# Performance work log

Measured on AMD Instinct MI355X. Metric: run time of the kernel, lower is better.

The kernel has to match this reference:

```python
import jax, jax.numpy as jnp
import numpy as np

HID, E, S, L_CAP, EPS = 768, 1536, 128, 512, 1e-5


def _rope_seq(x):
    """RoPE along axis 1. x: [b, n, 2, s]."""
    n, s = x.shape[1], x.shape[-1]
    half = s // 2
    inv_freq = jnp.power(10000.0, -jnp.arange(half, dtype=x.dtype) / half)  # [half]
    sinusoid = jnp.arange(n, dtype=x.dtype)[:, None, None] * inv_freq       # [n,1,half]
    sin, cos = jnp.sin(sinusoid), jnp.cos(sinusoid)
    x1, x2 = jnp.split(x, 2, axis=-1)
    return jnp.concatenate([x1 * cos - x2 * sin, x2 * cos + x1 * sin], axis=-1)


def setup_inputs() -> dict:
    key = jax.random.key(0)
    ks = jax.random.split(key, 6)
    B, L = 32, 512
    return {
        "x": jax.random.normal(ks[0], (B, L, HID), dtype=jnp.float32),
        "ln_gamma": jnp.ones((HID,), jnp.float32),
        "ln_beta": jnp.zeros((HID,), jnp.float32),
        "uv_W": jax.random.normal(ks[1], (HID, 2 * E + S), jnp.float32) * 0.02,
        "uv_b": jnp.zeros((2 * E + S,), jnp.float32),
        "gamma_qk": jax.random.normal(ks[2], (2, S), jnp.float32) * 0.02,
        "beta_qk": jnp.zeros((2, S), jnp.float32),
        "w_rel": jax.random.normal(ks[3], (2 * L_CAP - 1,), jnp.float32) * 0.02,
        "o_W": jax.random.normal(ks[4], (E, HID), jnp.float32) * 0.02,
        "o_b": jnp.zeros((HID,), jnp.float32),
    }


def reference(x, ln_gamma, ln_beta, uv_W, uv_b, gamma_qk, beta_qk, w_rel, o_W, o_b):
    L = x.shape[1]
    shortcut = x
    # LayerNorm
    mu = jnp.mean(x, axis=-1, keepdims=True)
    var = jnp.mean(jnp.square(x - mu), axis=-1, keepdims=True)
    xn = (x - mu) * jax.lax.rsqrt(var + EPS) * ln_gamma + ln_beta
    # uv projection + silu, split into u, v, base
    uv = jax.nn.silu(xn @ uv_W + uv_b)                       # [b, n, 2e+s]
    u, v, base = jnp.split(uv, [E, 2 * E], axis=-1)          # [b,n,e], [b,n,e], [b,n,s]
    # per-head affine then RoPE -> q, k
    base = base[..., None, :] * gamma_qk + beta_qk           # [b, n, 2, s]
    base = _rope_seq(base)
    q, k = base[..., 0, :], base[..., 1, :]
    # relu^2 attention kernel with Toeplitz relative position bias
    qk = jnp.einsum('bnd,bmd->bnm', q, k)
    idx = jnp.arange(L)
    bias = w_rel[idx[None, :] - idx[:, None] + L - 1]        # bias[i,j] = w[j-i+L-1]
    kernel = jnp.square(jax.nn.relu(qk / L + bias))
    # gated value aggregation + output projection + residual
    out = u * jnp.einsum('bnm,bme->bne', kernel, v)
    out = out @ o_W + o_b
    return out + shortcut
```

## Files before the change

kernel.cpp:

```cpp
#include <hip/hip_runtime.h>
#include <hip/hip_bf16.h>
#include <math.h>

typedef __bf16 bf16x8 __attribute__((ext_vector_type(8)));
typedef float f32x4 __attribute__((ext_vector_type(4)));
typedef unsigned short u16x4 __attribute__((ext_vector_type(4)));

#define AS1P const __attribute__((address_space(1))) void*
#define AS3P __attribute__((address_space(3))) void*

__device__ __forceinline__ float b2f(unsigned short h) {
    unsigned int u = ((unsigned int)h) << 16;
    return __builtin_bit_cast(float, u);
}
__device__ __forceinline__ unsigned short f2b(float f) {
    unsigned int u = __builtin_bit_cast(unsigned int, f);
    u += 0x7FFFu + ((u >> 16) & 1u);
    return (unsigned short)(u >> 16);
}
__device__ __forceinline__ float silu(float c) {
    return c * __builtin_amdgcn_rcpf(1.0f + __expf(-c));
}

__global__ __launch_bounds__(256) void k_convT(const float* __restrict__ src,
                                               unsigned short* __restrict__ dst,
                                               int R, int C) {
    __shared__ float tile[32][33];
    int tx = threadIdx.x, ty = threadIdx.y;
    int r0 = blockIdx.y << 5, c0 = blockIdx.x << 5;
#pragma unroll
    for (int i = 0; i < 4; ++i)
        tile[ty + 8 * i][tx] = src[(long long)(r0 + ty + 8 * i) * C + c0 + tx];
    __syncthreads();
#pragma unroll
    for (int i = 0; i < 4; ++i)
        dst[(long long)(c0 + ty + 8 * i) * R + r0 + tx] = f2b(tile[tx][ty + 8 * i]);
}

__global__ __launch_bounds__(256) void k_ln(const float* __restrict__ x,
                                            const float* __restrict__ g,
                                            const float* __restrict__ b,
                                            unsigned short* __restrict__ xn) {
    int row = blockIdx.x;
    int t = threadIdx.x;
    const float* xr = x + (long long)row * 768;
    float v0 = xr[t], v1 = xr[t + 256], v2 = xr[t + 512];
    float s = v0 + v1 + v2;
    float q = v0 * v0 + v1 * v1 + v2 * v2;
#pragma unroll
    for (int off = 32; off > 0; off >>= 1) {
        s += __shfl_xor(s, off);
        q += __shfl_xor(q, off);
    }
    __shared__ float ss[4], sq[4];
    int w = t >> 6;
    if ((t & 63) == 0) { ss[w] = s; sq[w] = q; }
    __syncthreads();
    float S_ = ss[0] + ss[1] + ss[2] + ss[3];
    float Q_ = sq[0] + sq[1] + sq[2] + sq[3];
    float mu = S_ * (1.0f / 768.0f);
    float var = Q_ * (1.0f / 768.0f) - mu * mu;
    float rs = rsqrtf(var + 1e-5f);
    unsigned short* xo = xn + (long long)row * 768;
    xo[t]       = f2b((v0 - mu) * rs * g[t]       + b[t]);
    xo[t + 256] = f2b((v1 - mu) * rs * g[t + 256] + b[t + 256]);
    xo[t + 512] = f2b((v2 - mu) * rs * g[t + 512] + b[t + 512]);
}

__global__ __launch_bounds__(128) void k_rope(const unsigned short* __restrict__ bS,
                                              const float* __restrict__ gqk,
                                              const float* __restrict__ bqk,
                                              unsigned short* __restrict__ q,
                                              unsigned short* __restrict__ k) {
    int row = blockIdx.x;
    int l = row & 511;
    int s = threadIdx.x;
    int j = s & 63;
    int partner = s ^ 64;
    float b0 = b2f(bS[(long long)row * 128 + s]);
    float bp = b2f(bS[(long long)row * 128 + partner]);
    float invf = __expf((float)j * -0.14391156831f);
    float th = (float)l * invf;
    float sn, cs;
    __sincosf(th, &sn, &cs);
    float sign = (s < 64) ? -1.0f : 1.0f;
    float preq  = b0 * gqk[s]           + bqk[s];
    float preqp = bp * gqk[partner]     + bqk[partner];
    q[(long long)row * 128 + s] = f2b(preq * cs + sign * preqp * sn);
    float prek  = b0 * gqk[128 + s]       + bqk[128 + s];
    float prekp = bp * gqk[128 + partner] + bqk[128 + partner];
    k[(long long)row * 128 + s] = f2b(prek * cs + sign * prekp * sn);
}

__global__ __launch_bounds__(256) void k_qk(const unsigned short* __restrict__ A,
                                            const unsigned short* __restrict__ B,
                                            const float* __restrict__ wrel,
                                            unsigned short* __restrict__ P) {
    __shared__ __align__(16) unsigned short As[128 * 64];
    __shared__ __align__(16) unsigned short Bs[128 * 64];
    int t = threadIdx.x;
    int w = t >> 6, lane = t & 63;
    int wr = w >> 1, wc = w & 1;
    int bx = blockIdx.x, by = blockIdx.y, bz = blockIdx.z;
    const unsigned short* Ab = A + (long long)bz * 512 * 128 + (long long)by * 128 * 128;
    const unsigned short* Bb = B + (long long)bz * 512 * 128 + (long long)bx * 128 * 128;

    f32x4 acc[4][4];
#pragma unroll
    for (int m = 0; m < 4; ++m)
#pragma unroll
        for (int n = 0; n < 4; ++n) acc[m][n] = (f32x4){0.f, 0.f, 0.f, 0.f};

    int rowA = (w << 3) + (lane >> 3);
    int colA = (lane & 7) << 3;

    for (int k0 = 0; k0 < 128; k0 += 64) {
#pragma unroll
        for (int i = 0; i < 4; ++i) {
            int r = (i << 5) + rowA;
            __builtin_amdgcn_global_load_lds(
                (AS1P)(Ab + (long long)r * 128 + k0 + colA),
                (AS3P)(&As[(i << 11) + (w << 9)]), 16, 0, 0);
            __builtin_amdgcn_global_load_lds(
                (AS1P)(Bb + (long long)r * 128 + k0 + colA),
                (AS3P)(&Bs[(i << 11) + (w << 9)]), 16, 0, 0);
        }
        __syncthreads();
#pragma unroll
        for (int ks = 0; ks < 2; ++ks) {
            bf16x8 af[4], bfr[4];
#pragma unroll
            for (int m = 0; m < 4; ++m)
                af[m] = *(const bf16x8*)&As[((wr << 6) + (m << 4) + (lane & 15)) * 64 +
                                            (ks << 5) + ((lane >> 4) << 3)];
#pragma unroll
            for (int n = 0; n < 4; ++n)
                bfr[n] = *(const bf16x8*)&Bs[((wc << 6) + (n << 4) + (lane & 15)) * 64 +
                                             (ks << 5) + ((lane >> 4) << 3)];
#pragma unroll
            for (int m = 0; m < 4; ++m)
#pragma unroll
                for (int n = 0; n < 4; ++n)
                    acc[m][n] = __builtin_amdgcn_mfma_f32_16x16x32_bf16(bfr[n], af[m],
                                                                        acc[m][n], 0, 0, 0);
        }
        __syncthreads();
    }

    int c15 = lane & 15, qq = lane >> 4;
    int rowb = (by << 7) + (wr << 6) + c15;
    int colb = (bx << 7) + (wc << 6) + (qq << 2);
#pragma unroll
    for (int m = 0; m < 4; ++m) {
#pragma unroll
        for (int n = 0; n < 4; ++n) {
            int grow = rowb + (m << 4);
            int gcol = colb + (n << 4);
            f32x4 a = acc[m][n];
            int base = gcol - grow + 511;
            u16x4 o;
#pragma unroll
            for (int i = 0; i < 4; ++i) {
                float val = a[i] * (1.0f / 512.0f) + wrel[base + i];
                val = fmaxf(val, 0.0f);
                o[i] = f2b(val * val);
            }
            *(u16x4*)(P + ((long long)(bz * 512 + grow)) * 512 + gcol) = o;
        }
    }
}

__device__ __forceinline__ bf16x8 ldsread(const unsigned short* p) {
    bf16x8 r;
    unsigned int off =
        (unsigned int)(unsigned long long)(__attribute__((address_space(3))) const void*)p;
    asm volatile("ds_read_b128 %0, %1" : "=v"(r) : "v"(off));
    return r;
}
__device__ __forceinline__ bf16x8 frag32(const unsigned short* tile, int r, int qq) {
    return ldsread(tile + r * 32 + ((qq ^ ((r >> 1) & 3)) << 3));
}
template <int ROWS, int K>
__device__ __forceinline__ void stage_t(const unsigned short* __restrict__ g,
                                        unsigned short* lds, int t) {
#pragma unroll
    for (int i = 0; i < ROWS / 64; ++i) {
        int slot = t + (i << 8);
        int row = slot >> 2;
        int gs = (slot & 3) ^ ((row >> 1) & 3);
        __builtin_amdgcn_global_load_lds(
            (AS1P)(g + (long long)row * K + (gs << 3)),
            (AS3P)(lds + slot * 8), 16, 0, 0);
    }
}

template <bool SWAP, int NT>
__device__ __forceinline__ void ring_kloop(const unsigned short* __restrict__ Ab,
                                           const unsigned short* __restrict__ Bb,
                                           unsigned short* As, unsigned short* Bs,
                                           f32x4 (&acc)[8][4], int t, int wc, int c15, int qq) {
    constexpr int K = NT * 32;
    constexpr int ASLOT = 128 * 32, BSLOT = 256 * 32;
    stage_t<128, K>(Ab, As, t);
    stage_t<256, K>(Bb, Bs, t);
    stage_t<128, K>(Ab + 32, As + ASLOT, t);
    stage_t<256, K>(Bb + 32, Bs + BSLOT, t);
    int slot = 0;
    for (int kt = 0; kt < NT; ++kt) {
        if (kt < NT - 1)
            asm volatile("s_waitcnt vmcnt(6)" ::: "memory");
        else
            asm volatile("s_waitcnt vmcnt(0)" ::: "memory");
        __builtin_amdgcn_s_barrier();
        __builtin_amdgcn_sched_barrier(0);
        if (kt + 2 < NT) {
            int ns = slot + 2;
            if (ns >= 3) ns -= 3;
            stage_t<128, K>(Ab + (long long)(kt + 2) * 32, As + ns * ASLOT, t);
            stage_t<256, K>(Bb + (long long)(kt + 2) * 32, Bs + ns * BSLOT, t);
        }
        const unsigned short* At = As + slot * ASLOT;
        const unsigned short* Bt = Bs + slot * BSLOT;
        bf16x8 af[8], bfr[4];
#pragma unroll
        for (int n = 0; n < 4; ++n) bfr[n] = frag32(Bt, wc * 64 + n * 16 + c15, qq);
#pragma unroll
        for (int m = 0; m < 8; ++m) af[m] = frag32(At, m * 16 + c15, qq);
        asm volatile("s_waitcnt lgkmcnt(0)" ::: "memory");
        __builtin_amdgcn_sched_barrier(0);
        __builtin_amdgcn_s_setprio(1);
#pragma unroll
        for (int m = 0; m < 8; ++m)
#pragma unroll
            for (int n = 0; n < 4; ++n) {
                if constexpr (SWAP)
                    acc[m][n] = __builtin_amdgcn_mfma_f32_16x16x32_bf16(bfr[n], af[m],
                                                                        acc[m][n], 0, 0, 0);
                else
                    acc[m][n] = __builtin_amdgcn_mfma_f32_16x16x32_bf16(af[m], bfr[n],
                                                                        acc[m][n], 0, 0, 0);
            }
        __builtin_amdgcn_s_setprio(0);
        slot = (slot + 1 == 3) ? 0 : slot + 1;
    }
}

template <int EPI, bool SWZ, int NT>
__global__ __launch_bounds__(256, 2) void k_ring(const unsigned short* __restrict__ A,
                                                 const unsigned short* __restrict__ B,
                                                 long long strideA, long long strideB,
                                                 void* p0, void* p1, void* p2,
                                                 const void* p3) {
    constexpr int K = NT * 32;
    __shared__ __align__(16) unsigned short As[3][128 * 32];
    __shared__ __align__(16) unsigned short Bs[3][256 * 32];
    int t = threadIdx.x;
    int w = t >> 6, lane = t & 63;
    int wc = w, c15 = lane & 15, qq = lane >> 4;
    int bx = blockIdx.x, by = blockIdx.y, bz = blockIdx.z;
    if constexpr (SWZ) {
        int gx = gridDim.x;
        int nb = gx * gridDim.y;
        int bid = by * gx + bx;
        int s = (bid & 7) * (nb >> 3) + (bid >> 3);
        bx = s % gx;
        by = s / gx;
    }
    const unsigned short* Ab = A + bz * strideA + (long long)by * 128 * K;
    const unsigned short* Bb = B + bz * strideB + (long long)bx * 256 * K;

    f32x4 acc[8][4];
#pragma unroll
    for (int m = 0; m < 8; ++m)
#pragma unroll
        for (int n = 0; n < 4; ++n) acc[m][n] = (f32x4){0.f, 0.f, 0.f, 0.f};

    bool swapped = true;
    if constexpr (EPI == 10) {
        swapped = !(bx >= 6 && bx < 12);
        if (swapped)
            ring_kloop<true, NT>(Ab, Bb, &As[0][0], &Bs[0][0], acc, t, wc, c15, qq);
        else
            ring_kloop<false, NT>(Ab, Bb, &As[0][0], &Bs[0][0], acc, t, wc, c15, qq);
    } else {
        ring_kloop<true, NT>(Ab, Bb, &As[0][0], &Bs[0][0], acc, t, wc, c15, qq);
    }

    if constexpr (EPI == 10) {
        if (swapped) {
            int rowb = by * 128 + c15;
            int colb = bx * 256 + wc * 64 + (qq << 2);
#pragma unroll
            for (int m = 0; m < 8; ++m) {
#pragma unroll
                for (int n = 0; n < 4; ++n) {
                    int R = rowb + m * 16;
                    int C = colb + n * 16;
                    f32x4 a = acc[m][n];
                    if (C < 1536) {
                        f32x4 bb = *(const f32x4*)((const float*)p3 + C);
                        u16x4 o;
#pragma unroll
                        for (int i = 0; i < 4; ++i) o[i] = f2b(silu(a[i] + bb[i]));
                        *(u16x4*)((unsigned short*)p0 + (long long)R * 1536 + C) = o;
                    } else if (C < 3200) {
                        f32x4 bb = *(const f32x4*)((const float*)p3 + C);
                        u16x4 o;
#pragma unroll
                        for (int i = 0; i < 4; ++i) o[i] = f2b(silu(a[i] + bb[i]));
                        *(u16x4*)((unsigned short*)p2 + (long long)R * 128 + (C - 3072)) = o;
                    }
                }
            }
        } else {
            int rowb = by * 128 + (qq << 2);
            int colb = bx * 256 + wc * 64 + c15;
#pragma unroll
            for (int m = 0; m < 8; ++m) {
#pragma unroll
                for (int n = 0; n < 4; ++n) {
                    int R = rowb + m * 16;
                    int C = colb + n * 16;
                    float bias = ((const float*)p3)[C];
                    f32x4 a = acc[m][n];
                    u16x4 o;
#pragma unroll
                    for (int i = 0; i < 4; ++i) o[i] = f2b(silu(a[i] + bias));
                    int bb2 = R >> 9, mm = R & 511;
                    *(u16x4*)((unsigned short*)p1 +
                              ((long long)bb2 * 1536 + (C - 1536)) * 512 + mm) = o;
                }
            }
        }
    } else if constexpr (EPI == 2) {
        int rowb = by * 128 + c15;
        int colb = bx * 256 + wc * 64 + (qq << 2);
#pragma unroll
        for (int m = 0; m < 8; ++m) {
#pragma unroll
            for (int n = 0; n < 4; ++n) {
                int R = rowb + m * 16;
                int C = colb + n * 16;
                f32x4 a = acc[m][n];
                long long idx = ((long long)(bz * 512 + R)) * 1536 + C;
                u16x4 uu = *(const u16x4*)((const unsigned short*)p1 + idx);
                u16x4 o;
#pragma unroll
                for (int i = 0; i < 4; ++i) o[i] = f2b(a[i] * b2f(uu[i]));
                *(u16x4*)((unsigned short*)p0 + idx) = o;
            }
        }
    } else {
        int rowb = by * 128 + c15;
        int colb = bx * 256 + wc * 64 + (qq << 2);
#pragma unroll
        for (int m = 0; m < 8; ++m) {
#pragma unroll
            for (int n = 0; n < 4; ++n) {
                int R = rowb + m * 16;
                int C = colb + n * 16;
                f32x4 a = acc[m][n];
                long long idx = (long long)R * 768 + C;
                f32x4 xv = *(const f32x4*)((const float*)p2 + idx);
                f32x4 ob = *(const f32x4*)((const float*)p1 + C);
                f32x4 o;
#pragma unroll
                for (int i = 0; i < 4; ++i) o[i] = a[i] + ob[i] + xv[i];
                *(f32x4*)((float*)p0 + idx) = o;
            }
        }
    }
}

extern "C" void kernel_launch(void* const* d_in, const int* in_sizes, int n_in,
                              void* d_out, int out_size, void* d_ws, size_t ws_size,
                              hipStream_t stream) {
    const float* x     = (const float*)d_in[0];
    const float* ln_g  = (const float*)d_in[1];
    const float* ln_b  = (const float*)d_in[2];
    const float* uv_W  = (const float*)d_in[3];
    const float* uv_b  = (const float*)d_in[4];
    const float* g_qk  = (const float*)d_in[5];
    const float* b_qk  = (const float*)d_in[6];
    const float* w_rel = (const float*)d_in[7];
    const float* o_W   = (const float*)d_in[8];
    const float* o_b   = (const float*)d_in[9];
    float* out = (float*)d_out;

    char* ws = (char*)d_ws;
    size_t off = 0;
    auto alloc = [&](size_t bytes) {
        void* p = ws + off;
        off += (bytes + 255) & ~(size_t)255;
        return p;
    };
    unsigned short* uvWT = (unsigned short*)alloc(3200ll * 768 * 2);
    unsigned short* oWT  = (unsigned short*)alloc(768ll * 1536 * 2);
    unsigned short* xn   = (unsigned short*)alloc(16384ll * 768 * 2);
    unsigned short* u    = (unsigned short*)alloc(16384ll * 1536 * 2);
    unsigned short* vT   = (unsigned short*)alloc(32ll * 1536 * 512 * 2);
    unsigned short* bS   = (unsigned short*)alloc(16384ll * 128 * 2);
    unsigned short* q    = (unsigned short*)alloc(32ll * 512 * 128 * 2);
    unsigned short* k    = (unsigned short*)alloc(32ll * 512 * 128 * 2);
    unsigned short* P     = xn;
    unsigned short* gated = u;

    k_convT<<<dim3(100, 24), dim3(32, 8), 0, stream>>>(uv_W, uvWT, 768, 3200);
    k_convT<<<dim3(24, 48), dim3(32, 8), 0, stream>>>(o_W, oWT, 1536, 768);
    k_ln<<<16384, 256, 0, stream>>>(x, ln_g, ln_b, xn);
    k_ring<10, true, 24><<<dim3(13, 128), 256, 0, stream>>>(
        xn, uvWT, 0, 0, (void*)u, (void*)vT, (void*)bS, (const void*)uv_b);
    k_rope<<<16384, 128, 0, stream>>>(bS, g_qk, b_qk, q, k);
    k_qk<<<dim3(4, 4, 32), 256, 0, stream>>>(q, k, w_rel, P);
    k_ring<2, false, 16><<<dim3(6, 4, 32), 256, 0, stream>>>(
        P, vT, 512ll * 512, 1536ll * 512, (void*)gated, (void*)u, nullptr, nullptr);
    k_ring<3, true, 48><<<dim3(3, 128), 256, 0, stream>>>(
        gated, oWT, 0, 0, (void*)out, (void*)o_b, (void*)x, nullptr);
}
```

Baseline: 296.7 us.

## Switch GEMMs to 256x256 tiles with 8 waves and half-tile double-buffered staging

Measured after the change: 291.8 us. About the same (-1.7%).

```diff
diff --git a/kernel.cpp b/kernel.cpp
--- a/kernel.cpp
+++ b/kernel.cpp
@@ -177,86 +177,115 @@
     asm volatile("ds_read_b128 %0, %1" : "=v"(r) : "v"(off));
     return r;
 }
-__device__ __forceinline__ bf16x8 frag32(const unsigned short* tile, int r, int qq) {
-    return ldsread(tile + r * 32 + ((qq ^ ((r >> 1) & 3)) << 3));
-}
-template <int ROWS, int K>
-__device__ __forceinline__ void stage_t(const unsigned short* __restrict__ g,
-                                        unsigned short* lds, int t) {
-#pragma unroll
-    for (int i = 0; i < ROWS / 64; ++i) {
-        int slot = t + (i << 8);
+__device__ __forceinline__ void stage_half(const unsigned short* __restrict__ g, int ldk,
+                                           unsigned short* lds, int t) {
+#pragma unroll
+    for (int i = 0; i < 2; ++i) {
+        int slot = t + (i << 9);
         int row = slot >> 2;
-        int gs = (slot & 3) ^ ((row >> 1) & 3);
+        int gs = (slot & 3) ^ ((slot >> 3) & 3);
         __builtin_amdgcn_global_load_lds(
-            (AS1P)(g + (long long)row * K + (gs << 3)),
+            (AS1P)(g + (long long)row * ldk + (gs << 3)),
             (AS3P)(lds + slot * 8), 16, 0, 0);
     }
 }
 
 template <bool SWAP, int NT>
-__device__ __forceinline__ void ring_kloop(const unsigned short* __restrict__ Ab,
-                                           const unsigned short* __restrict__ Bb,
-                                           unsigned short* As, unsigned short* Bs,
-                                           f32x4 (&acc)[8][4], int t, int wc, int c15, int qq) {
-    constexpr int K = NT * 32;
-    constexpr int ASLOT = 128 * 32, BSLOT = 256 * 32;
-    stage_t<128, K>(Ab, As, t);
-    stage_t<256, K>(Bb, Bs, t);
-    stage_t<128, K>(Ab + 32, As + ASLOT, t);
-    stage_t<256, K>(Bb + 32, Bs + BSLOT, t);
-    int slot = 0;
-    for (int kt = 0; kt < NT; ++kt) {
-        if (kt < NT - 1)
-            asm volatile("s_waitcnt vmcnt(6)" ::: "memory");
-        else
-            asm volatile("s_waitcnt vmcnt(0)" ::: "memory");
-        __builtin_amdgcn_s_barrier();
-        __builtin_amdgcn_sched_barrier(0);
-        if (kt + 2 < NT) {
-            int ns = slot + 2;
-            if (ns >= 3) ns -= 3;
-            stage_t<128, K>(Ab + (long long)(kt + 2) * 32, As + ns * ASLOT, t);
-            stage_t<256, K>(Bb + (long long)(kt + 2) * 32, Bs + ns * BSLOT, t);
-        }
-        const unsigned short* At = As + slot * ASLOT;
-        const unsigned short* Bt = Bs + slot * BSLOT;
-        bf16x8 af[8], bfr[4];
-#pragma unroll
-        for (int n = 0; n < 4; ++n) bfr[n] = frag32(Bt, wc * 64 + n * 16 + c15, qq);
-#pragma unroll
-        for (int m = 0; m < 8; ++m) af[m] = frag32(At, m * 16 + c15, qq);
-        asm volatile("s_waitcnt lgkmcnt(0)" ::: "memory");
-        __builtin_amdgcn_sched_barrier(0);
-        __builtin_amdgcn_s_setprio(1);
-#pragma unroll
-        for (int m = 0; m < 8; ++m)
-#pragma unroll
-            for (int n = 0; n < 4; ++n) {
-                if constexpr (SWAP)
-                    acc[m][n] = __builtin_amdgcn_mfma_f32_16x16x32_bf16(bfr[n], af[m],
-                                                                        acc[m][n], 0, 0, 0);
+__device__ __forceinline__ void kloop8(const unsigned short* __restrict__ Ab,
+                                       const unsigned short* __restrict__ Bb,
+                                       unsigned short* As, unsigned short* Bs,
+                                       f32x4 (&acc)[8][4], int tid,
+                                       int wr, int wc, int c15, int qq, int gq) {
+    constexpr int K = NT * 64;
+    stage_half(Ab, K, As + 0, tid);
+    stage_half(Bb, K, Bs + 0, tid);
+    stage_half(Ab + 32, K, As + 8192, tid);
+    stage_half(Bb + 32, K, Bs + 8192, tid);
+    stage_half(Ab + 64, K, As + 16384, tid);
+    stage_half(Bb + 64, K, Bs + 16384, tid);
+    asm volatile("s_waitcnt vmcnt(8)" ::: "memory");
+    __builtin_amdgcn_s_barrier();
+
+    bf16x8 bfr[4], af[4];
+    for (int t = 0; t < NT; ++t) {
+        const int b = t & 1;
+        const unsigned short* A0 = As + b * 16384;
+        const unsigned short* B0 = Bs + b * 16384;
+#pragma unroll
+        for (int p = 0; p < 4; ++p) {
+            const int ks = p >> 1, mh = p & 1;
+            const unsigned short* At = A0 + ks * 8192;
+            const unsigned short* Bt = B0 + ks * 8192;
+            if (mh == 0) {
+#pragma unroll
+                for (int n = 0; n < 4; ++n)
+                    bfr[n] = ldsread(Bt + (wc * 64 + n * 16 + c15) * 32 + gq * 8);
+            }
+#pragma unroll
+            for (int j = 0; j < 4; ++j)
+                af[j] = ldsread(At + (wr * 128 + (mh * 4 + j) * 16 + c15) * 32 + gq * 8);
+            if (p == 0) {
+                if (t + 1 < NT)
+                    stage_half(Ab + (t + 1) * 64 + 32, K,
+                               As + (((t + 1) & 1) * 2 + 1) * 8192, tid);
+            } else if (p == 1) {
+                if (t + 1 < NT)
+                    stage_half(Bb + (t + 1) * 64 + 32, K,
+                               Bs + (((t + 1) & 1) * 2 + 1) * 8192, tid);
+            } else if (p == 2) {
+                if (t + 2 < NT)
+                    stage_half(Ab + (t + 2) * 64, K, As + (b * 2) * 8192, tid);
+            } else {
+                if (t + 2 < NT)
+                    stage_half(Bb + (t + 2) * 64, K, Bs + (b * 2) * 8192, tid);
+            }
+            __builtin_amdgcn_s_barrier();
+            asm volatile("s_waitcnt lgkmcnt(0)" ::: "memory");
+            __builtin_amdgcn_sched_barrier(0);
+            __builtin_amdgcn_s_setprio(1);
+#pragma unroll
+            for (int j = 0; j < 4; ++j)
+#pragma unroll
+                for (int n = 0; n < 4; ++n) {
+                    if constexpr (SWAP)
+                        acc[mh * 4 + j][n] = __builtin_amdgcn_mfma_f32_16x16x32_bf16(
+                            bfr[n], af[j], acc[mh * 4 + j][n], 0, 0, 0);
+                    else
+                        acc[mh * 4 + j][n] = __builtin_amdgcn_mfma_f32_16x16x32_bf16(
+                            af[j], bfr[n], acc[mh * 4 + j][n], 0, 0, 0);
+                }
+            __builtin_amdgcn_s_setprio(0);
+            if (p == 1) {
+                if (t < NT - 1)
+                    asm volatile("s_waitcnt vmcnt(8)" ::: "memory");
                 else
-                    acc[m][n] = __builtin_amdgcn_mfma_f32_16x16x32_bf16(af[m], bfr[n],
-                                                                        acc[m][n], 0, 0, 0);
-            }
-        __builtin_amdgcn_s_setprio(0);
-        slot = (slot + 1 == 3) ? 0 : slot + 1;
+                    asm volatile("s_waitcnt vmcnt(0)" ::: "memory");
+            } else if (p == 3) {
+                if (t < NT - 2)
+                    asm volatile("s_waitcnt vmcnt(8)" ::: "memory");
+                else if (t == NT - 2)
+                    asm volatile("s_waitcnt vmcnt(4)" ::: "memory");
+            }
+            __builtin_amdgcn_sched_barrier(0);
+            __builtin_amdgcn_s_barrier();
+        }
     }
 }
 
 template <int EPI, bool SWZ, int NT>
-__global__ __launch_bounds__(256, 2) void k_ring(const unsigned short* __restrict__ A,
-                                                 const unsigned short* __restrict__ B,
-                                                 long long strideA, long long strideB,
-                                                 void* p0, void* p1, void* p2,
-                                                 const void* p3) {
-    constexpr int K = NT * 32;
-    __shared__ __align__(16) unsigned short As[3][128 * 32];
-    __shared__ __align__(16) unsigned short Bs[3][256 * 32];
-    int t = threadIdx.x;
-    int w = t >> 6, lane = t & 63;
-    int wc = w, c15 = lane & 15, qq = lane >> 4;
+__global__ __launch_bounds__(512, 2) void k8(const unsigned short* __restrict__ A,
+                                             const unsigned short* __restrict__ B,
+                                             long long strideA, long long strideB,
+                                             void* p0, void* p1, void* p2,
+                                             const void* p3) {
+    constexpr int K = NT * 64;
+    __shared__ __align__(16) unsigned short As[2][2][256 * 32];
+    __shared__ __align__(16) unsigned short Bs[2][2][256 * 32];
+    int tid = threadIdx.x;
+    int w = tid >> 6, lane = tid & 63;
+    int wr = w >> 2, wc = w & 3;
+    int c15 = lane & 15, qq = lane >> 4;
+    int gq = qq ^ ((c15 >> 1) & 3);
     int bx = blockIdx.x, by = blockIdx.y, bz = blockIdx.z;
     if constexpr (SWZ) {
         int gx = gridDim.x;
@@ -266,7 +295,7 @@
         bx = s % gx;
         by = s / gx;
     }
-    const unsigned short* Ab = A + bz * strideA + (long long)by * 128 * K;
+    const unsigned short* Ab = A + bz * strideA + (long long)by * 256 * K;
     const unsigned short* Bb = B + bz * strideB + (long long)bx * 256 * K;
 
     f32x4 acc[8][4];
@@ -279,16 +308,16 @@
     if constexpr (EPI == 10) {
         swapped = !(bx >= 6 && bx < 12);
         if (swapped)
-            ring_kloop<true, NT>(Ab, Bb, &As[0][0], &Bs[0][0], acc, t, wc, c15, qq);
+            kloop8<true, NT>(Ab, Bb, &As[0][0][0], &Bs[0][0][0], acc, tid, wr, wc, c15, qq, gq);
         else
-            ring_kloop<false, NT>(Ab, Bb, &As[0][0], &Bs[0][0], acc, t, wc, c15, qq);
+            kloop8<false, NT>(Ab, Bb, &As[0][0][0], &Bs[0][0][0], acc, tid, wr, wc, c15, qq, gq);
     } else {
-        ring_kloop<true, NT>(Ab, Bb, &As[0][0], &Bs[0][0], acc, t, wc, c15, qq);
+        kloop8<true, NT>(Ab, Bb, &As[0][0][0], &Bs[0][0][0], acc, tid, wr, wc, c15, qq, gq);
     }
 
     if constexpr (EPI == 10) {
         if (swapped) {
-            int rowb = by * 128 + c15;
+            int rowb = by * 256 + wr * 128 + c15;
             int colb = bx * 256 + wc * 64 + (qq << 2);
 #pragma unroll
             for (int m = 0; m < 8; ++m) {
@@ -313,7 +342,7 @@
                 }
             }
         } else {
-            int rowb = by * 128 + (qq << 2);
+            int rowb = by * 256 + wr * 128 + (qq << 2);
             int colb = bx * 256 + wc * 64 + c15;
 #pragma unroll
             for (int m = 0; m < 8; ++m) {
@@ -333,7 +362,7 @@
             }
         }
     } else if constexpr (EPI == 2) {
-        int rowb = by * 128 + c15;
+        int rowb = by * 256 + wr * 128 + c15;
         int colb = bx * 256 + wc * 64 + (qq << 2);
 #pragma unroll
         for (int m = 0; m < 8; ++m) {
@@ -351,7 +380,7 @@
             }
         }
     } else {
-        int rowb = by * 128 + c15;
+        int rowb = by * 256 + wr * 128 + c15;
         int colb = bx * 256 + wc * 64 + (qq << 2);
 #pragma unroll
         for (int m = 0; m < 8; ++m) {
@@ -394,7 +423,7 @@
         off += (bytes + 255) & ~(size_t)255;
         return p;
     };
-    unsigned short* uvWT = (unsigned short*)alloc(3200ll * 768 * 2);
+    unsigned short* uvWT = (unsigned short*)alloc(3328ll * 768 * 2);
     unsigned short* oWT  = (unsigned short*)alloc(768ll * 1536 * 2);
     unsigned short* xn   = (unsigned short*)alloc(16384ll * 768 * 2);
     unsigned short* u    = (unsigned short*)alloc(16384ll * 1536 * 2);
@@ -408,12 +437,12 @@
     k_convT<<<dim3(100, 24), dim3(32, 8), 0, stream>>>(uv_W, uvWT, 768, 3200);
     k_convT<<<dim3(24, 48), dim3(32, 8), 0, stream>>>(o_W, oWT, 1536, 768);
     k_ln<<<16384, 256, 0, stream>>>(x, ln_g, ln_b, xn);
-    k_ring<10, true, 24><<<dim3(13, 128), 256, 0, stream>>>(
+    k8<10, true, 12><<<dim3(13, 64), 512, 0, stream>>>(
         xn, uvWT, 0, 0, (void*)u, (void*)vT, (void*)bS, (const void*)uv_b);
     k_rope<<<16384, 128, 0, stream>>>(bS, g_qk, b_qk, q, k);
     k_qk<<<dim3(4, 4, 32), 256, 0, stream>>>(q, k, w_rel, P);
-    k_ring<2, false, 16><<<dim3(6, 4, 32), 256, 0, stream>>>(
+    k8<2, false, 8><<<dim3(6, 2, 32), 512, 0, stream>>>(
         P, vT, 512ll * 512, 1536ll * 512, (void*)gated, (void*)u, nullptr, nullptr);
-    k_ring<3, true, 48><<<dim3(3, 128), 256, 0, stream>>>(
+    k8<3, true, 24><<<dim3(3, 64), 512, 0, stream>>>(
         gated, oWT, 0, 0, (void*)out, (void*)o_b, (void*)x, nullptr);
 }
```

## Switch GEMMs to 256x256 tiles with 512 threads and interleaved LDS/MFMA pipeline

Applied to the files above, without the earlier changes.

New measurement: 293.8 us. Within noise of the previous version (-1.0%).

```diff
diff --git a/kernel.cpp b/kernel.cpp
--- a/kernel.cpp
+++ b/kernel.cpp
@@ -170,93 +170,121 @@
     }
 }
 
-__device__ __forceinline__ bf16x8 ldsread(const unsigned short* p) {
+__device__ __forceinline__ bf16x8 ldsb(const char* p) {
     bf16x8 r;
     unsigned int off =
         (unsigned int)(unsigned long long)(__attribute__((address_space(3))) const void*)p;
     asm volatile("ds_read_b128 %0, %1" : "=v"(r) : "v"(off));
     return r;
 }
-__device__ __forceinline__ bf16x8 frag32(const unsigned short* tile, int r, int qq) {
-    return ldsread(tile + r * 32 + ((qq ^ ((r >> 1) & 3)) << 3));
-}
-template <int ROWS, int K>
-__device__ __forceinline__ void stage_t(const unsigned short* __restrict__ g,
-                                        unsigned short* lds, int t) {
-#pragma unroll
-    for (int i = 0; i < ROWS / 64; ++i) {
-        int slot = t + (i << 8);
-        int row = slot >> 2;
-        int gs = (slot & 3) ^ ((row >> 1) & 3);
-        __builtin_amdgcn_global_load_lds(
-            (AS1P)(g + (long long)row * K + (gs << 3)),
-            (AS3P)(lds + slot * 8), 16, 0, 0);
-    }
+__device__ __forceinline__ void stage64(const unsigned short* __restrict__ g, int ldk,
+                                        char* lds, int r0, int w, int lane) {
+    int row = r0 + (w << 3) + (lane >> 3);
+    int colb = (lane & 7) << 4;
+    int scolb = colb ^ ((row & 7) << 4);
+    __builtin_amdgcn_global_load_lds(
+        (AS1P)((const char*)g + (long long)row * (ldk * 2) + scolb),
+        (AS3P)(lds + (r0 << 7) + (w << 10)), 16, 0, 0);
 }
 
 template <bool SWAP, int NT>
-__device__ __forceinline__ void ring_kloop(const unsigned short* __restrict__ Ab,
-                                           const unsigned short* __restrict__ Bb,
-                                           unsigned short* As, unsigned short* Bs,
-                                           f32x4 (&acc)[8][4], int t, int wc, int c15, int qq) {
-    constexpr int K = NT * 32;
-    constexpr int ASLOT = 128 * 32, BSLOT = 256 * 32;
-    stage_t<128, K>(Ab, As, t);
-    stage_t<256, K>(Bb, Bs, t);
-    stage_t<128, K>(Ab + 32, As + ASLOT, t);
-    stage_t<256, K>(Bb + 32, Bs + BSLOT, t);
-    int slot = 0;
-    for (int kt = 0; kt < NT; ++kt) {
-        if (kt < NT - 1)
-            asm volatile("s_waitcnt vmcnt(6)" ::: "memory");
-        else
-            asm volatile("s_waitcnt vmcnt(0)" ::: "memory");
-        __builtin_amdgcn_s_barrier();
-        __builtin_amdgcn_sched_barrier(0);
-        if (kt + 2 < NT) {
-            int ns = slot + 2;
-            if (ns >= 3) ns -= 3;
-            stage_t<128, K>(Ab + (long long)(kt + 2) * 32, As + ns * ASLOT, t);
-            stage_t<256, K>(Bb + (long long)(kt + 2) * 32, Bs + ns * BSLOT, t);
-        }
-        const unsigned short* At = As + slot * ASLOT;
-        const unsigned short* Bt = Bs + slot * BSLOT;
-        bf16x8 af[8], bfr[4];
-#pragma unroll
-        for (int n = 0; n < 4; ++n) bfr[n] = frag32(Bt, wc * 64 + n * 16 + c15, qq);
-#pragma unroll
-        for (int m = 0; m < 8; ++m) af[m] = frag32(At, m * 16 + c15, qq);
-        asm volatile("s_waitcnt lgkmcnt(0)" ::: "memory");
-        __builtin_amdgcn_sched_barrier(0);
-        __builtin_amdgcn_s_setprio(1);
-#pragma unroll
-        for (int m = 0; m < 8; ++m)
-#pragma unroll
-            for (int n = 0; n < 4; ++n) {
-                if constexpr (SWAP)
-                    acc[m][n] = __builtin_amdgcn_mfma_f32_16x16x32_bf16(bfr[n], af[m],
-                                                                        acc[m][n], 0, 0, 0);
-                else
-                    acc[m][n] = __builtin_amdgcn_mfma_f32_16x16x32_bf16(af[m], bfr[n],
-                                                                        acc[m][n], 0, 0, 0);
-            }
-        __builtin_amdgcn_s_setprio(0);
-        slot = (slot + 1 == 3) ? 0 : slot + 1;
-    }
+__device__ __forceinline__ void kloopP(const unsigned short* __restrict__ Ab,
+                                       const unsigned short* __restrict__ Bb,
+                                       char* A0, char* A1, char* B0, char* B1,
+                                       f32x4 (&acc)[8][4], int tid, int wr, int wc,
+                                       int o0, int o1) {
+    constexpr int K = NT * 64;
+    int w = tid >> 6, lane = tid & 63;
+    const int abase = wr * 16384;
+    const int bbase = wc * 8192;
+    bf16x8 afA[2], afB[2], bfrA[4], bfrB[4];
+
+#define STAGE(gA, gB, bufA, bufB)                          \
+    stage64(gA, K, bufA, 0, w, lane);                      \
+    stage64(gA, K, bufA, 64, w, lane);                     \
+    stage64(gA, K, bufA, 128, w, lane);                    \
+    stage64(gA, K, bufA, 192, w, lane);                    \
+    stage64(gB, K, bufB, 0, w, lane);                      \
+    stage64(gB, K, bufB, 64, w, lane);                     \
+    stage64(gB, K, bufB, 128, w, lane);                    \
+    stage64(gB, K, bufB, 192, w, lane);
+#define LA(DST, mp, OKS, BUF)                              \
+    DST[0] = ldsb((BUF) + abase + (mp) * 4096 + (OKS));    \
+    DST[1] = ldsb((BUF) + abase + (mp) * 4096 + 2048 + (OKS));
+#define LB(DST, OKS, BUF)                                  \
+    DST[0] = ldsb((BUF) + bbase + (OKS));                  \
+    DST[1] = ldsb((BUF) + bbase + 2048 + (OKS));           \
+    DST[2] = ldsb((BUF) + bbase + 4096 + (OKS));           \
+    DST[3] = ldsb((BUF) + bbase + 6144 + (OKS));
+#define WAITL(N)                                           \
+    asm volatile("s_waitcnt lgkmcnt(" #N ")" ::: "memory");\
+    __builtin_amdgcn_sched_barrier(0);
+#define MM(mp, BFR, AF)                                                               \
+    __builtin_amdgcn_s_setprio(1);                                                    \
+    _Pragma("unroll") for (int j_ = 0; j_ < 2; ++j_)                                  \
+        _Pragma("unroll") for (int n_ = 0; n_ < 4; ++n_) {                            \
+            if constexpr (SWAP)                                                       \
+                acc[(mp) * 2 + j_][n_] = __builtin_amdgcn_mfma_f32_16x16x32_bf16(     \
+                    BFR[n_], AF[j_], acc[(mp) * 2 + j_][n_], 0, 0, 0);                \
+            else                                                                      \
+                acc[(mp) * 2 + j_][n_] = __builtin_amdgcn_mfma_f32_16x16x32_bf16(     \
+                    AF[j_], BFR[n_], acc[(mp) * 2 + j_][n_], 0, 0, 0);                \
+        }                                                                             \
+    __builtin_amdgcn_s_setprio(0);
+#define TILE(CA, CB, NA, NB, t)                                                       \
+    LA(afB, 1, o0, CA) WAITL(2) MM(0, bfrA, afA)                                      \
+    LA(afA, 2, o0, CA) WAITL(2) MM(1, bfrA, afB)                                      \
+    LA(afB, 3, o0, CA) LB(bfrB, o1, CB) WAITL(6) MM(2, bfrA, afA)                     \
+    LA(afA, 0, o1, CA) WAITL(6) MM(3, bfrA, afB)                                      \
+    LA(afB, 1, o1, CA) WAITL(2) MM(0, bfrB, afA)                                      \
+    LA(afA, 2, o1, CA) WAITL(2) MM(1, bfrB, afB)                                      \
+    LA(afB, 3, o1, CA) WAITL(2) MM(2, bfrB, afA)                                      \
+    WAITL(0) MM(3, bfrB, afB)                                                         \
+    __builtin_amdgcn_s_barrier();                                                     \
+    if ((t) + 2 < NT) {                                                               \
+        STAGE(Ab + ((t) + 2) * 64, Bb + ((t) + 2) * 64, CA, CB)                       \
+        asm volatile("s_waitcnt vmcnt(8)" ::: "memory");                              \
+    } else if ((t) + 1 < NT) {                                                        \
+        asm volatile("s_waitcnt vmcnt(0)" ::: "memory");                              \
+    }                                                                                 \
+    __builtin_amdgcn_sched_barrier(0);                                                \
+    if ((t) + 1 < NT) { LB(bfrA, o0, NB) LA(afA, 0, o0, NA) }
+
+    STAGE(Ab, Bb, A0, B0)
+    STAGE(Ab + 64, Bb + 64, A1, B1)
+    asm volatile("s_waitcnt vmcnt(8)" ::: "memory");
+    __builtin_amdgcn_s_barrier();
+    LB(bfrA, o0, B0) LA(afA, 0, o0, A0)
+
+#pragma unroll 1
+    for (int t = 0; t < NT; t += 2) {
+        TILE(A0, B0, A1, B1, t)
+        TILE(A1, B1, A0, B0, t + 1)
+    }
+#undef STAGE
+#undef LA
+#undef LB
+#undef WAITL
+#undef MM
+#undef TILE
 }
 
 template <int EPI, bool SWZ, int NT>
-__global__ __launch_bounds__(256, 2) void k_ring(const unsigned short* __restrict__ A,
-                                                 const unsigned short* __restrict__ B,
-                                                 long long strideA, long long strideB,
-                                                 void* p0, void* p1, void* p2,
-                                                 const void* p3) {
-    constexpr int K = NT * 32;
-    __shared__ __align__(16) unsigned short As[3][128 * 32];
-    __shared__ __align__(16) unsigned short Bs[3][256 * 32];
-    int t = threadIdx.x;
-    int w = t >> 6, lane = t & 63;
-    int wc = w, c15 = lane & 15, qq = lane >> 4;
+__global__ __launch_bounds__(512, 2) void kP(const unsigned short* __restrict__ A,
+                                             const unsigned short* __restrict__ B,
+                                             long long strideA, long long strideB,
+                                             void* p0, void* p1, void* p2,
+                                             const void* p3) {
+    constexpr int K = NT * 64;
+    __shared__ __align__(16) char As[2][256 * 128];
+    __shared__ __align__(16) char Bs[2][256 * 128];
+    int tid = threadIdx.x;
+    int w = tid >> 6, lane = tid & 63;
+    int wr = w >> 2, wc = w & 3;
+    int c15 = lane & 15, qq = lane >> 4;
+    int g = (c15 & 7) << 4;
+    int o0 = c15 * 128 + ((qq * 16) ^ g);
+    int o1 = c15 * 128 + ((64 + qq * 16) ^ g);
     int bx = blockIdx.x, by = blockIdx.y, bz = blockIdx.z;
     if constexpr (SWZ) {
         int gx = gridDim.x;
@@ -266,7 +294,7 @@
         bx = s % gx;
         by = s / gx;
     }
-    const unsigned short* Ab = A + bz * strideA + (long long)by * 128 * K;
+    const unsigned short* Ab = A + bz * strideA + (long long)by * 256 * K;
     const unsigned short* Bb = B + bz * strideB + (long long)bx * 256 * K;
 
     f32x4 acc[8][4];
@@ -279,16 +307,16 @@
     if constexpr (EPI == 10) {
         swapped = !(bx >= 6 && bx < 12);
         if (swapped)
-            ring_kloop<true, NT>(Ab, Bb, &As[0][0], &Bs[0][0], acc, t, wc, c15, qq);
+            kloopP<true, NT>(Ab, Bb, As[0], As[1], Bs[0], Bs[1], acc, tid, wr, wc, o0, o1);
         else
-            ring_kloop<false, NT>(Ab, Bb, &As[0][0], &Bs[0][0], acc, t, wc, c15, qq);
+            kloopP<false, NT>(Ab, Bb, As[0], As[1], Bs[0], Bs[1], acc, tid, wr, wc, o0, o1);
     } else {
-        ring_kloop<true, NT>(Ab, Bb, &As[0][0], &Bs[0][0], acc, t, wc, c15, qq);
+        kloopP<true, NT>(Ab, Bb, As[0], As[1], Bs[0], Bs[1], acc, tid, wr, wc, o0, o1);
     }
 
     if constexpr (EPI == 10) {
         if (swapped) {
-            int rowb = by * 128 + c15;
+            int rowb = by * 256 + wr * 128 + c15;
             int colb = bx * 256 + wc * 64 + (qq << 2);
 #pragma unroll
             for (int m = 0; m < 8; ++m) {
@@ -313,7 +341,7 @@
                 }
             }
         } else {
-            int rowb = by * 128 + (qq << 2);
+            int rowb = by * 256 + wr * 128 + (qq << 2);
             int colb = bx * 256 + wc * 64 + c15;
 #pragma unroll
             for (int m = 0; m < 8; ++m) {
@@ -333,7 +361,7 @@
             }
         }
     } else if constexpr (EPI == 2) {
-        int rowb = by * 128 + c15;
+        int rowb = by * 256 + wr * 128 + c15;
         int colb = bx * 256 + wc * 64 + (qq << 2);
 #pragma unroll
         for (int m = 0; m < 8; ++m) {
@@ -351,7 +379,7 @@
             }
         }
     } else {
-        int rowb = by * 128 + c15;
+        int rowb = by * 256 + wr * 128 + c15;
         int colb = bx * 256 + wc * 64 + (qq << 2);
 #pragma unroll
         for (int m = 0; m < 8; ++m) {
@@ -394,7 +422,7 @@
         off += (bytes + 255) & ~(size_t)255;
         return p;
     };
-    unsigned short* uvWT = (unsigned short*)alloc(3200ll * 768 * 2);
+    unsigned short* uvWT = (unsigned short*)alloc(3328ll * 768 * 2);
     unsigned short* oWT  = (unsigned short*)alloc(768ll * 1536 * 2);
     unsigned short* xn   = (unsigned short*)alloc(16384ll * 768 * 2);
     unsigned short* u    = (unsigned short*)alloc(16384ll * 1536 * 2);
@@ -408,12 +436,12 @@
     k_convT<<<dim3(100, 24), dim3(32, 8), 0, stream>>>(uv_W, uvWT, 768, 3200);
     k_convT<<<dim3(24, 48), dim3(32, 8), 0, stream>>>(o_W, oWT, 1536, 768);
     k_ln<<<16384, 256, 0, stream>>>(x, ln_g, ln_b, xn);
-    k_ring<10, true, 24><<<dim3(13, 128), 256, 0, stream>>>(
+    kP<10, true, 12><<<dim3(13, 64), 512, 0, stream>>>(
         xn, uvWT, 0, 0, (void*)u, (void*)vT, (void*)bS, (const void*)uv_b);
     k_rope<<<16384, 128, 0, stream>>>(bS, g_qk, b_qk, q, k);
     k_qk<<<dim3(4, 4, 32), 256, 0, stream>>>(q, k, w_rel, P);
-    k_ring<2, false, 16><<<dim3(6, 4, 32), 256, 0, stream>>>(
+    kP<2, false, 8><<<dim3(6, 2, 32), 512, 0, stream>>>(
         P, vT, 512ll * 512, 1536ll * 512, (void*)gated, (void*)u, nullptr, nullptr);
-    k_ring<3, true, 48><<<dim3(3, 128), 256, 0, stream>>>(
+    kP<3, true, 24><<<dim3(3, 64), 512, 0, stream>>>(
         gated, oWT, 0, 0, (void*)out, (void*)o_b, (void*)x, nullptr);
 }
```

## Switch GEMM kernels to 128x128 tiles with 2x2 warps and double buffering

Applied to the files above, without the earlier changes.

Result: slower. 319.2 us (+7.6%).

```diff
diff --git a/kernel.cpp b/kernel.cpp
--- a/kernel.cpp
+++ b/kernel.cpp
@@ -180,57 +180,56 @@
 __device__ __forceinline__ bf16x8 frag32(const unsigned short* tile, int r, int qq) {
     return ldsread(tile + r * 32 + ((qq ^ ((r >> 1) & 3)) << 3));
 }
-template <int ROWS, int K>
-__device__ __forceinline__ void stage_t(const unsigned short* __restrict__ g,
-                                        unsigned short* lds, int t) {
-#pragma unroll
-    for (int i = 0; i < ROWS / 64; ++i) {
-        int slot = t + (i << 8);
-        int row = slot >> 2;
-        int gs = (slot & 3) ^ ((row >> 1) & 3);
+template <int K>
+__device__ __forceinline__ void stg128(const unsigned short* __restrict__ g,
+                                       unsigned short* lds, int t) {
+#pragma unroll
+    for (int i = 0; i < 2; ++i) {
+        int ch = t + (i << 8);
+        int row = ch >> 2;
+        int gs = (ch & 3) ^ ((row >> 1) & 3);
         __builtin_amdgcn_global_load_lds(
             (AS1P)(g + (long long)row * K + (gs << 3)),
-            (AS3P)(lds + slot * 8), 16, 0, 0);
+            (AS3P)(lds + ch * 8), 16, 0, 0);
     }
 }
 
 template <bool SWAP, int NT>
-__device__ __forceinline__ void ring_kloop(const unsigned short* __restrict__ Ab,
-                                           const unsigned short* __restrict__ Bb,
-                                           unsigned short* As, unsigned short* Bs,
-                                           f32x4 (&acc)[8][4], int t, int wc, int c15, int qq) {
+__device__ __forceinline__ void kloop4(const unsigned short* __restrict__ Ab,
+                                       const unsigned short* __restrict__ Bb,
+                                       unsigned short* As, unsigned short* Bs,
+                                       f32x4 (&acc)[4][4], int t, int wr, int wc,
+                                       int c15, int qq) {
     constexpr int K = NT * 32;
-    constexpr int ASLOT = 128 * 32, BSLOT = 256 * 32;
-    stage_t<128, K>(Ab, As, t);
-    stage_t<256, K>(Bb, Bs, t);
-    stage_t<128, K>(Ab + 32, As + ASLOT, t);
-    stage_t<256, K>(Bb + 32, Bs + BSLOT, t);
-    int slot = 0;
+    constexpr int SLOT = 128 * 32;
+    stg128<K>(Ab, As, t);
+    stg128<K>(Bb, Bs, t);
+    stg128<K>(Ab + 32, As + SLOT, t);
+    stg128<K>(Bb + 32, Bs + SLOT, t);
     for (int kt = 0; kt < NT; ++kt) {
         if (kt < NT - 1)
-            asm volatile("s_waitcnt vmcnt(6)" ::: "memory");
+            asm volatile("s_waitcnt vmcnt(4)" ::: "memory");
         else
             asm volatile("s_waitcnt vmcnt(0)" ::: "memory");
         __builtin_amdgcn_s_barrier();
         __builtin_amdgcn_sched_barrier(0);
-        if (kt + 2 < NT) {
-            int ns = slot + 2;
-            if (ns >= 3) ns -= 3;
-            stage_t<128, K>(Ab + (long long)(kt + 2) * 32, As + ns * ASLOT, t);
-            stage_t<256, K>(Bb + (long long)(kt + 2) * 32, Bs + ns * BSLOT, t);
-        }
-        const unsigned short* At = As + slot * ASLOT;
-        const unsigned short* Bt = Bs + slot * BSLOT;
-        bf16x8 af[8], bfr[4];
+        const unsigned short* At = As + (kt & 1) * SLOT;
+        const unsigned short* Bt = Bs + (kt & 1) * SLOT;
+        bf16x8 af[4], bfr[4];
+#pragma unroll
+        for (int m = 0; m < 4; ++m) af[m] = frag32(At, wr * 64 + m * 16 + c15, qq);
 #pragma unroll
         for (int n = 0; n < 4; ++n) bfr[n] = frag32(Bt, wc * 64 + n * 16 + c15, qq);
-#pragma unroll
-        for (int m = 0; m < 8; ++m) af[m] = frag32(At, m * 16 + c15, qq);
         asm volatile("s_waitcnt lgkmcnt(0)" ::: "memory");
         __builtin_amdgcn_sched_barrier(0);
+        __builtin_amdgcn_s_barrier();
+        if (kt + 2 < NT) {
+            stg128<K>(Ab + (long long)(kt + 2) * 32, As + (kt & 1) * SLOT, t);
+            stg128<K>(Bb + (long long)(kt + 2) * 32, Bs + (kt & 1) * SLOT, t);
+        }
         __builtin_amdgcn_s_setprio(1);
 #pragma unroll
-        for (int m = 0; m < 8; ++m)
+        for (int m = 0; m < 4; ++m)
 #pragma unroll
             for (int n = 0; n < 4; ++n) {
                 if constexpr (SWAP)
@@ -241,22 +240,22 @@
                                                                         acc[m][n], 0, 0, 0);
             }
         __builtin_amdgcn_s_setprio(0);
-        slot = (slot + 1 == 3) ? 0 : slot + 1;
     }
 }
 
 template <int EPI, bool SWZ, int NT>
-__global__ __launch_bounds__(256, 2) void k_ring(const unsigned short* __restrict__ A,
-                                                 const unsigned short* __restrict__ B,
-                                                 long long strideA, long long strideB,
-                                                 void* p0, void* p1, void* p2,
-                                                 const void* p3) {
+__global__ __launch_bounds__(256, 4) void k4(const unsigned short* __restrict__ A,
+                                             const unsigned short* __restrict__ B,
+                                             long long strideA, long long strideB,
+                                             void* p0, void* p1, void* p2,
+                                             const void* p3) {
     constexpr int K = NT * 32;
-    __shared__ __align__(16) unsigned short As[3][128 * 32];
-    __shared__ __align__(16) unsigned short Bs[3][256 * 32];
+    __shared__ __align__(16) unsigned short As[2][128 * 32];
+    __shared__ __align__(16) unsigned short Bs[2][128 * 32];
     int t = threadIdx.x;
     int w = t >> 6, lane = t & 63;
-    int wc = w, c15 = lane & 15, qq = lane >> 4;
+    int wr = w >> 1, wc = w & 1;
+    int c15 = lane & 15, qq = lane >> 4;
     int bx = blockIdx.x, by = blockIdx.y, bz = blockIdx.z;
     if constexpr (SWZ) {
         int gx = gridDim.x;
@@ -267,56 +266,51 @@
         by = s / gx;
     }
     const unsigned short* Ab = A + bz * strideA + (long long)by * 128 * K;
-    const unsigned short* Bb = B + bz * strideB + (long long)bx * 256 * K;
-
-    f32x4 acc[8][4];
-#pragma unroll
-    for (int m = 0; m < 8; ++m)
+    const unsigned short* Bb = B + bz * strideB + (long long)bx * 128 * K;
+
+    f32x4 acc[4][4];
+#pragma unroll
+    for (int m = 0; m < 4; ++m)
 #pragma unroll
         for (int n = 0; n < 4; ++n) acc[m][n] = (f32x4){0.f, 0.f, 0.f, 0.f};
 
     bool swapped = true;
     if constexpr (EPI == 10) {
-        swapped = !(bx >= 6 && bx < 12);
+        swapped = !(bx >= 12 && bx < 24);
         if (swapped)
-            ring_kloop<true, NT>(Ab, Bb, &As[0][0], &Bs[0][0], acc, t, wc, c15, qq);
+            kloop4<true, NT>(Ab, Bb, &As[0][0], &Bs[0][0], acc, t, wr, wc, c15, qq);
         else
-            ring_kloop<false, NT>(Ab, Bb, &As[0][0], &Bs[0][0], acc, t, wc, c15, qq);
+            kloop4<false, NT>(Ab, Bb, &As[0][0], &Bs[0][0], acc, t, wr, wc, c15, qq);
     } else {
-        ring_kloop<true, NT>(Ab, Bb, &As[0][0], &Bs[0][0], acc, t, wc, c15, qq);
+        kloop4<true, NT>(Ab, Bb, &As[0][0], &Bs[0][0], acc, t, wr, wc, c15, qq);
     }
 
     if constexpr (EPI == 10) {
         if (swapped) {
-            int rowb = by * 128 + c15;
-            int colb = bx * 256 + wc * 64 + (qq << 2);
-#pragma unroll
-            for (int m = 0; m < 8; ++m) {
+            int rowb = by * 128 + wr * 64 + c15;
+            int colb = bx * 128 + wc * 64 + (qq << 2);
+#pragma unroll
+            for (int m = 0; m < 4; ++m) {
 #pragma unroll
                 for (int n = 0; n < 4; ++n) {
                     int R = rowb + m * 16;
                     int C = colb + n * 16;
                     f32x4 a = acc[m][n];
-                    if (C < 1536) {
-                        f32x4 bb = *(const f32x4*)((const float*)p3 + C);
-                        u16x4 o;
-#pragma unroll
-                        for (int i = 0; i < 4; ++i) o[i] = f2b(silu(a[i] + bb[i]));
+                    f32x4 bb = *(const f32x4*)((const float*)p3 + C);
+                    u16x4 o;
+#pragma unroll
+                    for (int i = 0; i < 4; ++i) o[i] = f2b(silu(a[i] + bb[i]));
+                    if (C < 1536)
                         *(u16x4*)((unsigned short*)p0 + (long long)R * 1536 + C) = o;
-                    } else if (C < 3200) {
-                        f32x4 bb = *(const f32x4*)((const float*)p3 + C);
-                        u16x4 o;
-#pragma unroll
-                        for (int i = 0; i < 4; ++i) o[i] = f2b(silu(a[i] + bb[i]));
+                    else
                         *(u16x4*)((unsigned short*)p2 + (long long)R * 128 + (C - 3072)) = o;
-                    }
                 }
             }
         } else {
-            int rowb = by * 128 + (qq << 2);
-            int colb = bx * 256 + wc * 64 + c15;
-#pragma unroll
-            for (int m = 0; m < 8; ++m) {
+            int rowb = by * 128 + wr * 64 + (qq << 2);
+            int colb = bx * 128 + wc * 64 + c15;
+#pragma unroll
+            for (int m = 0; m < 4; ++m) {
 #pragma unroll
                 for (int n = 0; n < 4; ++n) {
                     int R = rowb + m * 16;
@@ -333,10 +327,10 @@
             }
         }
     } else if constexpr (EPI == 2) {
-        int rowb = by * 128 + c15;
-        int colb = bx * 256 + wc * 64 + (qq << 2);
-#pragma unroll
-        for (int m = 0; m < 8; ++m) {
+        int rowb = by * 128 + wr * 64 + c15;
+        int colb = bx * 128 + wc * 64 + (qq << 2);
+#pragma unroll
+        for (int m = 0; m < 4; ++m) {
 #pragma unroll
             for (int n = 0; n < 4; ++n) {
                 int R = rowb + m * 16;
@@ -351,10 +345,10 @@
             }
         }
     } else {
-        int rowb = by * 128 + c15;
-        int colb = bx * 256 + wc * 64 + (qq << 2);
-#pragma unroll
-        for (int m = 0; m < 8; ++m) {
+        int rowb = by * 128 + wr * 64 + c15;
+        int colb = bx * 128 + wc * 64 + (qq << 2);
+#pragma unroll
+        for (int m = 0; m < 4; ++m) {
 #pragma unroll
             for (int n = 0; n < 4; ++n) {
                 int R = rowb + m * 16;
@@ -408,12 +402,12 @@
     k_convT<<<dim3(100, 24), dim3(32, 8), 0, stream>>>(uv_W, uvWT, 768, 3200);
     k_convT<<<dim3(24, 48), dim3(32, 8), 0, stream>>>(o_W, oWT, 1536, 768);
     k_ln<<<16384, 256, 0, stream>>>(x, ln_g, ln_b, xn);
-    k_ring<10, true, 24><<<dim3(13, 128), 256, 0, stream>>>(
+    k4<10, true, 24><<<dim3(25, 128), 256, 0, stream>>>(
         xn, uvWT, 0, 0, (void*)u, (void*)vT, (void*)bS, (const void*)uv_b);
     k_rope<<<16384, 128, 0, stream>>>(bS, g_qk, b_qk, q, k);
     k_qk<<<dim3(4, 4, 32), 256, 0, stream>>>(q, k, w_rel, P);
-    k_ring<2, false, 16><<<dim3(6, 4, 32), 256, 0, stream>>>(
+    k4<2, false, 16><<<dim3(12, 4, 32), 256, 0, stream>>>(
         P, vT, 512ll * 512, 1536ll * 512, (void*)gated, (void*)u, nullptr, nullptr);
-    k_ring<3, true, 48><<<dim3(3, 128), 256, 0, stream>>>(
+    k4<3, true, 48><<<dim3(6, 128), 256, 0, stream>>>(
         gated, oWT, 0, 0, (void*)out, (void*)o_b, (void*)x, nullptr);
 }
```
